# Kernel tuning notes

Measured on AMD Instinct MI355X. Metric: run time of the kernel, lower is better.

Reference implementation:

```python
import jax, jax.numpy as jnp
import numpy as np

L = 512          # angles_max_length
R_CA = 3.8       # C-alpha - C-alpha virtual bond length (AB model)


def _B_mat(a, b):
    # Rigid transform of the AB C-alpha model: rot(alpha) about z, rot(beta), translate R along x.
    ca, sa = jnp.cos(a), jnp.sin(a)
    cb, sb = jnp.cos(b), jnp.sin(b)
    z = jnp.zeros_like(a)
    o = jnp.ones_like(a)
    rows = [
        [ca, -sa * cb,  sa * sb, R_CA * ca],
        [sa,  ca * cb, -ca * sb, R_CA * sa],
        [z,   sb,       cb,      z],
        [z,   z,        z,       o],
    ]
    return jnp.stack([jnp.stack(r, -1) for r in rows], -2)  # (..., 4, 4)


def _dB_da(a, b):
    ca, sa = jnp.cos(a), jnp.sin(a)
    cb, sb = jnp.cos(b), jnp.sin(b)
    z = jnp.zeros_like(a)
    rows = [
        [-sa, -ca * cb,  ca * sb, -R_CA * sa],
        [ ca, -sa * cb,  sa * sb,  R_CA * ca],
        [z, z, z, z],
        [z, z, z, z],
    ]
    return jnp.stack([jnp.stack(r, -1) for r in rows], -2)


def _dB_db(a, b):
    ca, sa = jnp.cos(a), jnp.sin(a)
    cb, sb = jnp.cos(b), jnp.sin(b)
    z = jnp.zeros_like(a)
    rows = [
        [z,  sa * sb,  sa * cb, z],
        [z, -ca * sb, -ca * cb, z],
        [z,  cb,      -sb,      z],
        [z, z, z, z],
    ]
    return jnp.stack([jnp.stack(r, -1) for r in rows], -2)


def setup_inputs() -> dict:
    key = jax.random.key(0)
    k1, k2, k3 = jax.random.split(key, 3)
    input_angles = jax.random.normal(k1, (32, 2, L), dtype=jnp.float32)
    input_coords = jax.random.normal(k2, (32, 3 * (L + 1)), dtype=jnp.float32)
    angles_length = jax.random.randint(k3, (32,), 0, L, dtype=jnp.int32)
    return {"input_angles": input_angles, "input_coords": input_coords,
            "angles_length": angles_length}


def reference(input_angles, input_coords, angles_length):
    Bsz = input_angles.shape[0]
    alpha = input_angles[:, 0, :]  # (B, L)
    beta = input_angles[:, 1, :]

    Bm = _B_mat(alpha, beta)  # (B, L, 4, 4)
    # Prefix products M_i = B_0 @ ... @ B_i (order-preserving associative scan).
    M = jax.lax.associative_scan(lambda x, y: x @ y, Bm, axis=1)
    eye = jnp.broadcast_to(jnp.eye(4, dtype=Bm.dtype), (Bsz, 1, 4, 4))
    M_prev = jnp.concatenate([eye, M[:, :-1]], axis=1)  # M_{i-1}

    # Rigid-transform inverse of M_i: [R^T, -R^T t; 0 1]
    Rm = M[..., :3, :3]
    t = M[..., :3, 3:]
    Rt = jnp.swapaxes(Rm, -1, -2)
    bottom = jnp.broadcast_to(jnp.array([0., 0., 0., 1.], Bm.dtype), (Bsz, L, 1, 4))
    Minv = jnp.concatenate(
        [jnp.concatenate([Rt, -(Rt @ t)], axis=-1), bottom], axis=-2)

    # F_i^q = M_{i-1} dB_i/dq M_i^{-1};  dr_j/dq_i = F_i^q r_j^h  (for j > i)
    Fa = M_prev @ _dB_da(alpha, beta) @ Minv  # (B, L, 4, 4)
    Fb = M_prev @ _dB_db(alpha, beta) @ Minv

    coords = input_coords.reshape(Bsz, L + 1, 3)
    rh = jnp.concatenate([coords, jnp.ones((Bsz, L + 1, 1), coords.dtype)], -1)

    ga = jnp.einsum('blij,bmj->blmi', Fa, rh)[..., :3]  # (B, L, L+1, 3)
    gb = jnp.einsum('blij,bmj->blmi', Fb, rh)[..., :3]

    i = jnp.arange(L)[:, None]
    j = jnp.arange(L + 1)[None, :]
    lens = angles_length[:, None, None]
    mask = ((j > i) & (i < lens) & (j <= lens))[..., None]
    ga = jnp.where(mask, ga, 0.0)
    gb = jnp.where(mask, gb, 0.0)

    out = jnp.stack([ga, gb], axis=1)  # (B, 2, L, L+1, 3)
    return out.reshape(Bsz, 2, 3 * L * (L + 1))
```

## Files before the change

### kernel.cpp

```cpp
#include <hip/hip_runtime.h>

#define LSEQ 512
#define RCA 3.8f

struct Aff { float m[3][4]; };

__device__ __forceinline__ Aff compose(const Aff& A, const Aff& B) {
    Aff C;
#pragma unroll
    for (int i = 0; i < 3; ++i) {
#pragma unroll
        for (int j = 0; j < 4; ++j) {
            float v = A.m[i][0] * B.m[0][j] + A.m[i][1] * B.m[1][j] + A.m[i][2] * B.m[2][j];
            if (j == 3) v += A.m[i][3];
            C.m[i][j] = v;
        }
    }
    return C;
}

__device__ __forceinline__ Aff shflUp(const Aff& a, int d) {
    Aff r;
#pragma unroll
    for (int i = 0; i < 3; ++i)
#pragma unroll
        for (int j = 0; j < 4; ++j)
            r.m[i][j] = __shfl_up(a.m[i][j], d, 64);
    return r;
}

__device__ __forceinline__ Aff makeB(float ca, float sa, float cb, float sb) {
    Aff B;
    B.m[0][0] = ca;  B.m[0][1] = -sa * cb; B.m[0][2] =  sa * sb; B.m[0][3] = RCA * ca;
    B.m[1][0] = sa;  B.m[1][1] =  ca * cb; B.m[1][2] = -ca * sb; B.m[1][3] = RCA * sa;
    B.m[2][0] = 0.f; B.m[2][1] =  sb;      B.m[2][2] =  cb;      B.m[2][3] = 0.f;
    return B;
}

__global__ __launch_bounds__(512) void scan_kernel(const float* __restrict__ angles,
                                                   float* __restrict__ F) {
    const int b = blockIdx.x;
    const int tid = threadIdx.x;
    const int lane = tid & 63;
    const int w = tid >> 6;

    __shared__ float sT[8][12];

    const float a  = angles[(size_t)b * 1024 + tid];
    const float be = angles[(size_t)b * 1024 + 512 + tid];
    float sa, ca, sb, cb;
    sincosf(a, &sa, &ca);
    sincosf(be, &sb, &cb);

    Aff S = makeB(ca, sa, cb, sb);
#pragma unroll
    for (int d = 1; d < 64; d <<= 1) {
        Aff o = shflUp(S, d);
        if (lane >= d) S = compose(o, S);
    }

    if (lane == 63) {
#pragma unroll
        for (int k = 0; k < 12; ++k) sT[w][k] = S.m[k / 4][k % 4];
    }
    __syncthreads();

    Aff E;
#pragma unroll
    for (int i = 0; i < 3; ++i)
#pragma unroll
        for (int j = 0; j < 4; ++j) E.m[i][j] = (i == j) ? 1.f : 0.f;
    for (int k = 0; k < w; ++k) {
        Aff T;
#pragma unroll
        for (int q = 0; q < 12; ++q) T.m[q / 4][q % 4] = sT[k][q];
        E = compose(E, T);
    }

    const Aff Sp = shflUp(S, 1);
    const Aff M = compose(E, S);
    Aff Mprev;
    if (lane == 0) Mprev = E;
    else           Mprev = compose(E, Sp);

    float Rt[3][3], ti[3];
#pragma unroll
    for (int i = 0; i < 3; ++i)
#pragma unroll
        for (int j = 0; j < 3; ++j) Rt[i][j] = M.m[j][i];
#pragma unroll
    for (int i = 0; i < 3; ++i)
        ti[i] = -(M.m[0][i] * M.m[0][3] + M.m[1][i] * M.m[1][3] + M.m[2][i] * M.m[2][3]);

    float d0[4] = {-sa, -ca * cb,  ca * sb, -RCA * sa};
    float d1[4] = { ca, -sa * cb,  sa * sb,  RCA * ca};
    float e01 =  sa * sb, e02 =  sa * cb;
    float e11 = -ca * sb, e12 = -ca * cb;
    float e21 =  cb,      e22 = -sb;

    float Ga[3][4], Gb[3][4];
#pragma unroll
    for (int i = 0; i < 3; ++i) {
        float p0 = Mprev.m[i][0], p1 = Mprev.m[i][1], p2 = Mprev.m[i][2];
#pragma unroll
        for (int j = 0; j < 4; ++j) Ga[i][j] = p0 * d0[j] + p1 * d1[j];
        Gb[i][0] = 0.f;
        Gb[i][1] = p0 * e01 + p1 * e11 + p2 * e21;
        Gb[i][2] = p0 * e02 + p1 * e12 + p2 * e22;
        Gb[i][3] = 0.f;
    }

    float W[24];
#pragma unroll
    for (int i = 0; i < 3; ++i) {
#pragma unroll
        for (int j = 0; j < 3; ++j) {
            W[i * 4 + j]      = Ga[i][0] * Rt[0][j] + Ga[i][1] * Rt[1][j] + Ga[i][2] * Rt[2][j];
            W[12 + i * 4 + j] = Gb[i][0] * Rt[0][j] + Gb[i][1] * Rt[1][j] + Gb[i][2] * Rt[2][j];
        }
        W[i * 4 + 3]      = Ga[i][0] * ti[0] + Ga[i][1] * ti[1] + Ga[i][2] * ti[2] + Ga[i][3];
        W[12 + i * 4 + 3] = Gb[i][0] * ti[0] + Gb[i][1] * ti[1] + Gb[i][2] * ti[2] + Gb[i][3];
    }

    float4* w4 = reinterpret_cast<float4*>(F + ((size_t)b * LSEQ + tid) * 24);
    const float4* s4 = reinterpret_cast<const float4*>(W);
#pragma unroll
    for (int q = 0; q < 6; ++q) w4[q] = s4[q];
}

__global__ __launch_bounds__(256) void emit_kernel(const float* __restrict__ F,
                                                   const float* __restrict__ coords,
                                                   const int* __restrict__ lens,
                                                   float* __restrict__ out) {
    const int b = blockIdx.y;
    const int l0 = blockIdx.x * 4;
    const int tid = threadIdx.x;

    __shared__ float sF[96];
    if (tid < 96) sF[tid] = F[((size_t)b * LSEQ + l0) * 24 + tid];
    __syncthreads();

    const int len = lens[b];
    const float* cp = coords + (size_t)b * 1539;

    const int m0 = tid, m1 = tid + 256, m2 = tid + 512;
    const float cx0 = cp[m0 * 3], cy0 = cp[m0 * 3 + 1], cz0 = cp[m0 * 3 + 2];
    const float cx1 = cp[m1 * 3], cy1 = cp[m1 * 3 + 1], cz1 = cp[m1 * 3 + 2];
    const bool has2 = (m2 < 513);
    float cx2 = 0.f, cy2 = 0.f, cz2 = 0.f;
    if (has2) { cx2 = cp[m2 * 3]; cy2 = cp[m2 * 3 + 1]; cz2 = cp[m2 * 3 + 2]; }

#pragma unroll
    for (int i = 0; i < 4; ++i) {
        const int l = l0 + i;
        const float* f = sF + i * 24;
        const float f00 = f[0],  f01 = f[1],  f02 = f[2],  f03 = f[3];
        const float f10 = f[4],  f11 = f[5],  f12 = f[6],  f13 = f[7];
        const float f20 = f[8],  f21 = f[9],  f22 = f[10], f23 = f[11];
        const float g00 = f[12], g01 = f[13], g02 = f[14], g03 = f[15];
        const float g10 = f[16], g11 = f[17], g12 = f[18], g13 = f[19];
        const float g20 = f[20], g21 = f[21], g22 = f[22], g23 = f[23];

        const size_t baseA = ((size_t)(b * 2) * LSEQ + l) * 1539;
        const size_t baseB = baseA + (size_t)LSEQ * 1539;
        const bool rowActive = (l < len);

        auto emit1 = [&](int m, float x, float y, float z) {
            const float s = (rowActive && (m > l) && (m <= len)) ? 1.f : 0.f;
            float3 va, vb;
            va.x = s * (f00 * x + f01 * y + f02 * z + f03);
            va.y = s * (f10 * x + f11 * y + f12 * z + f13);
            va.z = s * (f20 * x + f21 * y + f22 * z + f23);
            vb.x = s * (g00 * x + g01 * y + g02 * z + g03);
            vb.y = s * (g10 * x + g11 * y + g12 * z + g13);
            vb.z = s * (g20 * x + g21 * y + g22 * z + g23);
            *reinterpret_cast<float3*>(out + baseA + (size_t)m * 3) = va;
            *reinterpret_cast<float3*>(out + baseB + (size_t)m * 3) = vb;
        };

        emit1(m0, cx0, cy0, cz0);
        emit1(m1, cx1, cy1, cz1);
        if (has2) emit1(m2, cx2, cy2, cz2);
    }
}

extern "C" void kernel_launch(void* const* d_in, const int* in_sizes, int n_in,
                              void* d_out, int out_size, void* d_ws, size_t ws_size,
                              hipStream_t stream) {
    const float* angles = (const float*)d_in[0];
    const float* coords = (const float*)d_in[1];
    const int*   lens   = (const int*)d_in[2];
    float* out = (float*)d_out;
    float* F = (float*)d_ws;

    scan_kernel<<<32, 512, 0, stream>>>(angles, F);
    emit_kernel<<<dim3(128, 32), 256, 0, stream>>>(F, coords, lens, out);
}
```

Before: 205.9 us.

## Emit one row per block with aligned 16-byte nontemporal stores

The emit kernel now gives each block a single (batch, row) pair and walks the flattened row of 1539 floats in aligned 4-float quads. Each element's point and component are found with a multiply-shift division by three. Coordinates and the row's F matrix go into LDS only when the row is active; inactive rows just write zeros. The aim is to replace the misaligned 12-byte float3 stores with aligned 16-byte nontemporal stores, in exchange for four times more blocks and per-element index arithmetic.

After: 228.0 us. 10.7% more time.

```diff
diff --git a/kernel.cpp b/kernel.cpp
--- a/kernel.cpp
+++ b/kernel.cpp
@@ -2,6 +2,8 @@
 
 #define LSEQ 512
 #define RCA 3.8f
+
+typedef float f32x4 __attribute__((ext_vector_type(4)));
 
 struct Aff { float m[3][4]; };
 
@@ -122,8 +124,8 @@
         W[12 + i * 4 + 3] = Gb[i][0] * ti[0] + Gb[i][1] * ti[1] + Gb[i][2] * ti[2] + Gb[i][3];
     }
 
-    float4* w4 = reinterpret_cast<float4*>(F + ((size_t)b * LSEQ + tid) * 24);
-    const float4* s4 = reinterpret_cast<const float4*>(W);
+    f32x4* w4 = reinterpret_cast<f32x4*>(F + ((size_t)b * LSEQ + tid) * 24);
+    const f32x4* s4 = reinterpret_cast<const f32x4*>(W);
 #pragma unroll
     for (int q = 0; q < 6; ++q) w4[q] = s4[q];
 }
@@ -132,56 +134,60 @@
                                                    const float* __restrict__ coords,
                                                    const int* __restrict__ lens,
                                                    float* __restrict__ out) {
+    const int l = blockIdx.x;
     const int b = blockIdx.y;
-    const int l0 = blockIdx.x * 4;
     const int tid = threadIdx.x;
-
-    __shared__ float sF[96];
-    if (tid < 96) sF[tid] = F[((size_t)b * LSEQ + l0) * 24 + tid];
-    __syncthreads();
-
-    const int len = lens[b];
-    const float* cp = coords + (size_t)b * 1539;
-
-    const int m0 = tid, m1 = tid + 256, m2 = tid + 512;
-    const float cx0 = cp[m0 * 3], cy0 = cp[m0 * 3 + 1], cz0 = cp[m0 * 3 + 2];
-    const float cx1 = cp[m1 * 3], cy1 = cp[m1 * 3 + 1], cz1 = cp[m1 * 3 + 2];
-    const bool has2 = (m2 < 513);
-    float cx2 = 0.f, cy2 = 0.f, cz2 = 0.f;
-    if (has2) { cx2 = cp[m2 * 3]; cy2 = cp[m2 * 3 + 1]; cz2 = cp[m2 * 3 + 2]; }
-
-#pragma unroll
-    for (int i = 0; i < 4; ++i) {
-        const int l = l0 + i;
-        const float* f = sF + i * 24;
-        const float f00 = f[0],  f01 = f[1],  f02 = f[2],  f03 = f[3];
-        const float f10 = f[4],  f11 = f[5],  f12 = f[6],  f13 = f[7];
-        const float f20 = f[8],  f21 = f[9],  f22 = f[10], f23 = f[11];
-        const float g00 = f[12], g01 = f[13], g02 = f[14], g03 = f[15];
-        const float g10 = f[16], g11 = f[17], g12 = f[18], g13 = f[19];
-        const float g20 = f[20], g21 = f[21], g22 = f[22], g23 = f[23];
-
-        const size_t baseA = ((size_t)(b * 2) * LSEQ + l) * 1539;
-        const size_t baseB = baseA + (size_t)LSEQ * 1539;
-        const bool rowActive = (l < len);
-
-        auto emit1 = [&](int m, float x, float y, float z) {
-            const float s = (rowActive && (m > l) && (m <= len)) ? 1.f : 0.f;
-            float3 va, vb;
-            va.x = s * (f00 * x + f01 * y + f02 * z + f03);
-            va.y = s * (f10 * x + f11 * y + f12 * z + f13);
-            va.z = s * (f20 * x + f21 * y + f22 * z + f23);
-            vb.x = s * (g00 * x + g01 * y + g02 * z + g03);
-            vb.y = s * (g10 * x + g11 * y + g12 * z + g13);
-            vb.z = s * (g20 * x + g21 * y + g22 * z + g23);
-            *reinterpret_cast<float3*>(out + baseA + (size_t)m * 3) = va;
-            *reinterpret_cast<float3*>(out + baseB + (size_t)m * 3) = vb;
-        };
-
-        emit1(m0, cx0, cy0, cz0);
-        emit1(m1, cx1, cy1, cz1);
-        if (has2) emit1(m2, cx2, cy2, cz2);
-    }
+    int len = lens[b];
+    if (len > 511) len = 511;
+    const bool rowActive = (l < len);
+
+    __shared__ float sC[1536];
+    __shared__ float sF[24];
+
+    const size_t rowA_elem = ((size_t)(b * 2) * LSEQ + l) * 1539;
+    const size_t rowB_elem = rowA_elem + (size_t)LSEQ * 1539;
+    float* __restrict__ rowA = out + rowA_elem;
+    float* __restrict__ rowB = out + rowB_elem;
+    const int h = (int)((4 - (rowA_elem & 3)) & 3);
+
+    if (rowActive) {
+        const float* cp = coords + (size_t)b * 1539;
+        for (int k = tid; k < 1536; k += 256) sC[k] = cp[k];
+        if (tid < 24) sF[tid] = F[((size_t)b * LSEQ + l) * 24 + tid];
+        __syncthreads();
+    }
+
+    if (tid < h)     { rowA[tid] = 0.f;            rowB[tid] = 0.f; }
+    if (tid < 3 - h) { rowA[h + 1536 + tid] = 0.f; rowB[h + 1536 + tid] = 0.f; }
+
+    const int eLo = 3 * (l + 1);
+    const int eHi = 3 * len + 2;
+
+    auto doQuad = [&](int q) {
+        const int p = h + 4 * q;
+        f32x4 va = {0.f, 0.f, 0.f, 0.f};
+        f32x4 vb = {0.f, 0.f, 0.f, 0.f};
+        if (rowActive && (p + 3 >= eLo) && (p <= eHi)) {
+#pragma unroll
+            for (int j = 0; j < 4; ++j) {
+                const int e = p + j;
+                const int m = (e * 43691) >> 17;
+                const int c = e - 3 * m;
+                if (m > l && m <= len) {
+                    const float x = sC[3 * m], y = sC[3 * m + 1], z = sC[3 * m + 2];
+                    const float* fa = sF + c * 4;
+                    const float* fb = fa + 12;
+                    va[j] = fa[0] * x + fa[1] * y + fa[2] * z + fa[3];
+                    vb[j] = fb[0] * x + fb[1] * y + fb[2] * z + fb[3];
+                }
+            }
+        }
+        __builtin_nontemporal_store(va, reinterpret_cast<f32x4*>(rowA + p));
+        __builtin_nontemporal_store(vb, reinterpret_cast<f32x4*>(rowB + p));
+    };
+
+    doQuad(tid);
+    if (tid < 128) doQuad(tid + 256);
 }
 
 extern "C" void kernel_launch(void* const* d_in, const int* in_sizes, int n_in,
@@ -194,5 +200,5 @@
     float* F = (float*)d_ws;
 
     scan_kernel<<<32, 512, 0, stream>>>(angles, F);
-    emit_kernel<<<dim3(128, 32), 256, 0, stream>>>(F, coords, lens, out);
-}
+    emit_kernel<<<dim3(512, 32), 256, 0, stream>>>(F, coords, lens, out);
+}
```
